# Kernel tuning notes

Hardware: AMD Instinct MI355X
Metric: run time of the kernel (lower is better)

The kernel has to match this reference:

```python
import jax, jax.numpy as jnp
import numpy as np

# Polynomial coefficients from the original module (hard-coded in forward).
P00, P10, P20, P30 = 0.0, 0.0, 0.0, 0.0      # identity-kernel branch (all zero)
P01, P11, P21 = -0.000287, 0.266, -0.1097    # learned-weight branch
STRIDE, PAD = 1, 1


def _conv(x, w):
    # NCHW input, OIHW kernel -> NCHW output. Equivalent to
    # unfold(x).T @ w.view(O,-1).T reshaped back, i.e. torch's im2col matmul.
    return jax.lax.conv_general_dilated(
        x, w,
        window_strides=(STRIDE, STRIDE),
        padding=[(PAD, PAD), (PAD, PAD)],
        dimension_numbers=('NCHW', 'OIHW', 'NCHW'))


def setup_inputs() -> dict:
    key = jax.random.key(0)
    k1, k2 = jax.random.split(key)
    img = jax.random.normal(k1, (16, 64, 128, 128), dtype=jnp.float32)
    # weights initialized N(0, 0.8) in the original module
    weights = jax.random.normal(k2, (64, 64, 3, 3), dtype=jnp.float32) * 0.8
    identity_kernel = jnp.ones((64, 64, 3, 3), dtype=jnp.float32)
    return {"img": img, "weights": weights, "identity_kernel": identity_kernel}


def reference(img, weights, identity_kernel):
    kh, kw = weights.shape[2], weights.shape[3]
    # Elementwise polynomial applied to the input, then contracted against
    # the (identity, learned) kernels. matmul-with-unfold == convolution,
    # so we express it as two convs instead of materializing im2col.
    poly_id = P00 + P10 * img + P20 * img**2 + P30 * img**3  # == zeros here
    poly_w = P01 + P11 * img + P21 * img**2
    out = _conv(poly_id, identity_kernel) + _conv(poly_w, weights)
    return out / (3 * kh * kw)
```

## Files before the change

kernel.cpp:

```cpp
#include <hip/hip_runtime.h>


typedef __bf16 bf16;
typedef __attribute__((ext_vector_type(8))) __bf16 bf16x8;
typedef __attribute__((ext_vector_type(16))) float f32x16;

static constexpr float A0 = -0.000287f / 27.0f;
static constexpr float A1 =  0.266f    / 27.0f;
static constexpr float A2 = -0.1097f   / 27.0f;

#define NN 16
#define CI 64
#define HH 128
#define WW 128
#define OO 64
#define LDS_BYTES 74112

__global__ void repack_w(const float* __restrict__ w, bf16* __restrict__ wrb) {
    int idx = blockIdx.x * 256 + threadIdx.x;
    if (idx >= 9 * 8 * 64 * 8) return;
    int cj    = idx & 7;
    int o     = (idx >> 3) & 63;
    int cc8   = (idx >> 9) & 7;
    int slice = idx >> 12;
    int ky = slice / 3, kx = slice - ky * 3;
    int c = cc8 * 8 + cj;
    wrb[idx] = (bf16)w[((o * CI + c) * 3 + ky) * 3 + kx];
}

__global__ __launch_bounds__(512, 4) void conv_mfma(const float* __restrict__ img,
                                                    const bf16* __restrict__ wrb,
                                                    float* __restrict__ out) {
    extern __shared__ __align__(16) char smem[];
    float* slots = (float*)smem;
    bf16*  ilds  = (bf16*)(smem + 49152);

    const int tid = threadIdx.x;
    const int b   = blockIdx.x;
    const int y0  = (b & 31) * 4;
    const int n   = b >> 5;

    const int wv   = tid >> 6;
    const int lane = tid & 63;
    const int lm   = lane & 31;
    const int half = lane >> 5;
    const int yl   = wv >> 1;
    const int Xh   = (wv & 1) * 64;

    auto dma = [&](int h, int i0, int i1) {
        float* slot = slots + (h & 1) * 6144;
        const int cb = h * 8;
        for (int i = i0; i < i1; ++i) {
            const int q   = wv + 8 * i;
            const int r   = q >> 2;
            const int ch0 = (2 * q) & 7;
            const int yi  = y0 - 1 + r;
            if ((unsigned)yi < 128u) {
                const float* g = img + ((n * CI + cb + ch0 + half) * HH + yi) * WW + lm * 4;
                __builtin_amdgcn_global_load_lds(
                    (const __attribute__((address_space(1))) void*)g,
                    (__attribute__((address_space(3))) void*)(slot + q * 256),
                    16, 0, 0);
            }
        }
    };

    auto transform = [&](int h) {
        const float* slot = slots + (h & 1) * 6144;
        const int ccl = h & 1;
        if (tid < 390) {
            const int r  = tid / 65;
            const int xh = tid - r * 65;
            const int yi = y0 - 1 + r;
            bf16* rowp = ilds + (r * 2 + ccl) * (130 * 8);
            if (xh < 64) {
                bf16x8 pk0, pk1;
                if ((unsigned)yi < 128u) {
                    const float* p = slot + (r * 8) * 128 + 2 * xh;
                    #pragma unroll
                    for (int j = 0; j < 8; ++j) {
                        float2 v = *(const float2*)(p + j * 128);
                        pk0[j] = (bf16)(A0 + v.x * (A1 + A2 * v.x));
                        pk1[j] = (bf16)(A0 + v.y * (A1 + A2 * v.y));
                    }
                } else {
                    #pragma unroll
                    for (int j = 0; j < 8; ++j) { pk0[j] = (bf16)0.0f; pk1[j] = (bf16)0.0f; }
                }
                *(bf16x8*)(rowp + (2 * xh + 1) * 8) = pk0;
                *(bf16x8*)(rowp + (2 * xh + 2) * 8) = pk1;
            } else {
                bf16x8 z;
                #pragma unroll
                for (int j = 0; j < 8; ++j) z[j] = (bf16)0.0f;
                *(bf16x8*)(rowp + 0) = z;
                *(bf16x8*)(rowp + 129 * 8) = z;
            }
        }
    };

    f32x16 acc[2][2];
    #pragma unroll
    for (int i = 0; i < 2; ++i)
        #pragma unroll
        for (int j = 0; j < 2; ++j)
            #pragma unroll
            for (int k = 0; k < 16; ++k) acc[i][j][k] = 0.0f;

    const bf16x8* wfr = (const bf16x8*)wrb;
    const bf16x8* ifr = (const bf16x8*)ilds;

    dma(0, 0, 3);

    for (int h = 0; h < 8; ++h) {
        __syncthreads();
        if (h < 7) dma(h + 1, 0, 2);
        transform(h);
        if (h & 1) {
            __syncthreads();
            if (h < 7) dma(h + 1, 2, 3);
            const int cc8g = (h >> 1) * 2 + half;
            #pragma unroll
            for (int ky = 0; ky < 3; ++ky) {
                const int r = yl + ky;
                #pragma unroll
                for (int kx = 0; kx < 3; ++kx) {
                    const int slice = ky * 3 + kx;
                    bf16x8 a0 = wfr[(slice * 8 + cc8g) * 64 + lm];
                    bf16x8 a1 = wfr[(slice * 8 + cc8g) * 64 + 32 + lm];
                    const int ib = (r * 2 + half) * 130 + Xh + lm + kx;
                    bf16x8 b0 = ifr[ib];
                    bf16x8 b1 = ifr[ib + 32];
                    acc[0][0] = __builtin_amdgcn_mfma_f32_32x32x16_bf16(a0, b0, acc[0][0], 0, 0, 0);
                    acc[0][1] = __builtin_amdgcn_mfma_f32_32x32x16_bf16(a0, b1, acc[0][1], 0, 0, 0);
                    acc[1][0] = __builtin_amdgcn_mfma_f32_32x32x16_bf16(a1, b0, acc[1][0], 0, 0, 0);
                    acc[1][1] = __builtin_amdgcn_mfma_f32_32x32x16_bf16(a1, b1, acc[1][1], 0, 0, 0);
                }
            }
        } else {
            if (h < 7) dma(h + 1, 2, 3);
        }
    }

    const int ybase = (n * OO * HH + (y0 + yl)) * WW;
    #pragma unroll
    for (int p = 0; p < 2; ++p)
        #pragma unroll
        for (int xt = 0; xt < 2; ++xt) {
            const int x = Xh + xt * 32 + lm;
            #pragma unroll
            for (int rg = 0; rg < 16; ++rg) {
                const int o = (rg & 3) + 8 * (rg >> 2) + 4 * half + 32 * p;
                out[ybase + o * (HH * WW) + x] = acc[p][xt][rg];
            }
        }
}

extern "C" void kernel_launch(void* const* d_in, const int* in_sizes, int n_in,
                              void* d_out, int out_size, void* d_ws, size_t ws_size,
                              hipStream_t stream) {
    const float* img = (const float*)d_in[0];
    const float* w   = (const float*)d_in[1];
    float* out = (float*)d_out;
    bf16* wrb  = (bf16*)d_ws;

    static bool attr_done = false;
    if (!attr_done) {
        (void)hipFuncSetAttribute((const void*)conv_mfma,
                                  hipFuncAttributeMaxDynamicSharedMemorySize, LDS_BYTES);
        attr_done = true;
    }

    repack_w<<<(9 * 8 * 64 * 8 + 255) / 256, 256, 0, stream>>>(w, wrb);
    conv_mfma<<<NN * (HH / 4), 512, LDS_BYTES, stream>>>(img, wrb, out);
}
```

Measured before the change: 134.1 us.

## Stage weights in LDS and pipeline input in finer four-channel chunks

Restructures the main loop into 16 smaller stages of four channels each, with half-size double-buffered input slots. It replaces __syncthreads with explicit vmcnt waits plus s_barrier so one batch of async loads can stay in flight. Weights are now DMA'd into LDS per 16-channel chunk in a new layout instead of being read from global memory inside the MFMA loop. The goals are to cut LDS footprint, overlap global loads with the transform, and avoid global-memory latency on weight fragments. The cost is more barriers per block, and hand-tuned waitcnt values that are fragile.

```diff
diff --git a/kernel.cpp b/kernel.cpp
--- a/kernel.cpp
+++ b/kernel.cpp
@@ -2,6 +2,7 @@
 
 
 typedef __bf16 bf16;
+typedef __attribute__((ext_vector_type(4))) __bf16 bf16x4;
 typedef __attribute__((ext_vector_type(8))) __bf16 bf16x8;
 typedef __attribute__((ext_vector_type(16))) float f32x16;
 
@@ -14,17 +15,18 @@
 #define HH 128
 #define WW 128
 #define OO 64
-#define LDS_BYTES 74112
+#define LDS_BYTES 67968
 
 __global__ void repack_w(const float* __restrict__ w, bf16* __restrict__ wrb) {
     int idx = blockIdx.x * 256 + threadIdx.x;
-    if (idx >= 9 * 8 * 64 * 8) return;
-    int cj    = idx & 7;
-    int o     = (idx >> 3) & 63;
-    int cc8   = (idx >> 9) & 7;
-    int slice = idx >> 12;
-    int ky = slice / 3, kx = slice - ky * 3;
-    int c = cc8 * 8 + cj;
+    if (idx >= 36864) return;
+    int c16 = idx & 15;
+    int o   = (idx >> 4) & 63;
+    int sc  = idx >> 10;
+    int ch  = sc / 9;
+    int s   = sc - ch * 9;
+    int ky = s / 3, kx = s - ky * 3;
+    int c = ch * 16 + c16;
     wrb[idx] = (bf16)w[((o * CI + c) * 3 + ky) * 3 + kx];
 }
 
@@ -33,7 +35,8 @@
                                                     float* __restrict__ out) {
     extern __shared__ __align__(16) char smem[];
     float* slots = (float*)smem;
-    bf16*  ilds  = (bf16*)(smem + 49152);
+    bf16*  ilds  = (bf16*)(smem + 24576);
+    bf16*  wlds  = (bf16*)(smem + 49536);
 
     const int tid = threadIdx.x;
     const int b   = blockIdx.x;
@@ -47,54 +50,68 @@
     const int yl   = wv >> 1;
     const int Xh   = (wv & 1) * 64;
 
-    auto dma = [&](int h, int i0, int i1) {
-        float* slot = slots + (h & 1) * 6144;
-        const int cb = h * 8;
-        for (int i = i0; i < i1; ++i) {
-            const int q   = wv + 8 * i;
-            const int r   = q >> 2;
-            const int ch0 = (2 * q) & 7;
-            const int yi  = y0 - 1 + r;
-            if ((unsigned)yi < 128u) {
-                const float* g = img + ((n * CI + cb + ch0 + half) * HH + yi) * WW + lm * 4;
-                __builtin_amdgcn_global_load_lds(
-                    (const __attribute__((address_space(1))) void*)g,
-                    (__attribute__((address_space(3))) void*)(slot + q * 256),
-                    16, 0, 0);
-            }
+    auto idma = [&](int q) {
+        float* slot = slots + (q & 1) * 3072;
+        const int cbase = (q >> 2) * 16 + (q & 3) * 4;
+        #pragma unroll
+        for (int k = 0; k < 2; ++k) {
+            const int u  = (k == 0) ? wv : (wv < 4 ? 8 + wv : wv);
+            const int r  = u >> 1;
+            const int cp = u & 1;
+            int yi = y0 - 1 + r;
+            yi = yi < 0 ? 0 : (yi > 127 ? 127 : yi);
+            const float* g = img + ((n * CI + cbase + 2 * cp + (lane >> 5)) * HH + yi) * WW
+                           + 4 * (lane & 31);
+            __builtin_amdgcn_global_load_lds(
+                (const __attribute__((address_space(1))) void*)g,
+                (__attribute__((address_space(3))) void*)(slot + u * 256),
+                16, 0, 0);
         }
     };
 
-    auto transform = [&](int h) {
-        const float* slot = slots + (h & 1) * 6144;
-        const int ccl = h & 1;
+    auto wdma = [&](int c) {
+        #pragma unroll
+        for (int k = 0; k < 3; ++k) {
+            const int u = (k == 0) ? wv : (k == 1 ? 8 + wv : (wv < 2 ? 16 + wv : wv));
+            const bf16* g = wrb + c * 9216 + u * 512 + lane * 8;
+            __builtin_amdgcn_global_load_lds(
+                (const __attribute__((address_space(1))) void*)g,
+                (__attribute__((address_space(3))) void*)(wlds + u * 512),
+                16, 0, 0);
+        }
+    };
+
+    auto transform = [&](int q) {
+        const float* slot = slots + (q & 1) * 3072;
+        const int ccl = (q & 3) >> 1;
+        const int cj4 = (q & 1) * 4;
         if (tid < 390) {
             const int r  = tid / 65;
             const int xh = tid - r * 65;
             const int yi = y0 - 1 + r;
-            bf16* rowp = ilds + (r * 2 + ccl) * (130 * 8);
+            bf16* rowp = ilds + (r * 2 + ccl) * (130 * 8) + cj4;
             if (xh < 64) {
-                bf16x8 pk0, pk1;
+                bf16x4 pk0, pk1;
                 if ((unsigned)yi < 128u) {
-                    const float* p = slot + (r * 8) * 128 + 2 * xh;
                     #pragma unroll
-                    for (int j = 0; j < 8; ++j) {
-                        float2 v = *(const float2*)(p + j * 128);
+                    for (int j = 0; j < 4; ++j) {
+                        float2 v = *(const float2*)(slot + (r * 2 + (j >> 1)) * 256
+                                                    + (j & 1) * 128 + 2 * xh);
                         pk0[j] = (bf16)(A0 + v.x * (A1 + A2 * v.x));
                         pk1[j] = (bf16)(A0 + v.y * (A1 + A2 * v.y));
                     }
                 } else {
                     #pragma unroll
-                    for (int j = 0; j < 8; ++j) { pk0[j] = (bf16)0.0f; pk1[j] = (bf16)0.0f; }
+                    for (int j = 0; j < 4; ++j) { pk0[j] = (bf16)0.0f; pk1[j] = (bf16)0.0f; }
                 }
-                *(bf16x8*)(rowp + (2 * xh + 1) * 8) = pk0;
-                *(bf16x8*)(rowp + (2 * xh + 2) * 8) = pk1;
+                *(bf16x4*)(rowp + (2 * xh + 1) * 8) = pk0;
+                *(bf16x4*)(rowp + (2 * xh + 2) * 8) = pk1;
             } else {
-                bf16x8 z;
+                bf16x4 z;
                 #pragma unroll
-                for (int j = 0; j < 8; ++j) z[j] = (bf16)0.0f;
-                *(bf16x8*)(rowp + 0) = z;
-                *(bf16x8*)(rowp + 129 * 8) = z;
+                for (int j = 0; j < 4; ++j) z[j] = (bf16)0.0f;
+                *(bf16x4*)(rowp + 0) = z;
+                *(bf16x4*)(rowp + 129 * 8) = z;
             }
         }
     };
@@ -107,27 +124,31 @@
             #pragma unroll
             for (int k = 0; k < 16; ++k) acc[i][j][k] = 0.0f;
 
-    const bf16x8* wfr = (const bf16x8*)wrb;
-    const bf16x8* ifr = (const bf16x8*)ilds;
+    idma(0);
 
-    dma(0, 0, 3);
-
-    for (int h = 0; h < 8; ++h) {
-        __syncthreads();
-        if (h < 7) dma(h + 1, 0, 2);
-        transform(h);
-        if (h & 1) {
-            __syncthreads();
-            if (h < 7) dma(h + 1, 2, 3);
-            const int cc8g = (h >> 1) * 2 + half;
+    for (int q = 0; q < 16; ++q) {
+        if ((q & 3) == 1) asm volatile("s_waitcnt vmcnt(3)" ::: "memory");
+        else              asm volatile("s_waitcnt vmcnt(0)" ::: "memory");
+        __builtin_amdgcn_sched_barrier(0);
+        __builtin_amdgcn_s_barrier();
+        __builtin_amdgcn_sched_barrier(0);
+        if (q < 15) idma(q + 1);
+        if ((q & 3) == 0) wdma(q >> 2);
+        transform(q);
+        if ((q & 3) == 3) {
+            asm volatile("s_waitcnt lgkmcnt(0)" ::: "memory");
+            __builtin_amdgcn_sched_barrier(0);
+            __builtin_amdgcn_s_barrier();
+            __builtin_amdgcn_sched_barrier(0);
+            const bf16x8* ifr = (const bf16x8*)ilds;
             #pragma unroll
             for (int ky = 0; ky < 3; ++ky) {
                 const int r = yl + ky;
                 #pragma unroll
                 for (int kx = 0; kx < 3; ++kx) {
                     const int slice = ky * 3 + kx;
-                    bf16x8 a0 = wfr[(slice * 8 + cc8g) * 64 + lm];
-                    bf16x8 a1 = wfr[(slice * 8 + cc8g) * 64 + 32 + lm];
+                    bf16x8 a0 = *(const bf16x8*)(wlds + (slice * 64 + lm) * 16 + half * 8);
+                    bf16x8 a1 = *(const bf16x8*)(wlds + (slice * 64 + 32 + lm) * 16 + half * 8);
                     const int ib = (r * 2 + half) * 130 + Xh + lm + kx;
                     bf16x8 b0 = ifr[ib];
                     bf16x8 b1 = ifr[ib + 32];
@@ -137,8 +158,6 @@
                     acc[1][1] = __builtin_amdgcn_mfma_f32_32x32x16_bf16(a1, b1, acc[1][1], 0, 0, 0);
                 }
             }
-        } else {
-            if (h < 7) dma(h + 1, 2, 3);
         }
     }
 
@@ -171,6 +190,6 @@
         attr_done = true;
     }
 
-    repack_w<<<(9 * 8 * 64 * 8 + 255) / 256, 256, 0, stream>>>(w, wrb);
+    repack_w<<<(36864 + 255) / 256, 256, 0, stream>>>(w, wrb);
     conv_mfma<<<NN * (HH / 4), 512, LDS_BYTES, stream>>>(img, wrb, out);
 }
```

After: 134.2 us. About the same (+0.1%).
